# Kernel tuning notes

Hardware: AMD Instinct MI355X
Metric: run time of the kernel (lower is better)

## Reference

```python
import jax, jax.numpy as jnp
import numpy as np

S = 16   # num_states
C = 8    # input_channels
B = 64   # batch
L = 4096 # sequence length


def hyperbolic_sigmoid(x):
    return x / (1 + jnp.abs(x)) * 0.5 + 0.5


def hyperbolic_softmax(logits, axis):
    x = hyperbolic_sigmoid(logits)
    return x / jnp.sum(x, axis=axis, keepdims=True)


def setup_inputs() -> dict:
    key = jax.random.key(0)
    k0, k1, k2, k3 = jax.random.split(key, 4)
    return {
        "log_input_probs": jax.random.normal(k0, (B, L, C), dtype=jnp.float32),
        "invh_initial_state_probs": jax.random.normal(k1, (S,), dtype=jnp.float32),
        "invh_transition_probs": jax.random.normal(k2, (S, C, S), dtype=jnp.float32),
        "invh_accepting_state_probs": jax.random.normal(k3, (S,), dtype=jnp.float32),
    }


def reference(log_input_probs, invh_initial_state_probs, invh_transition_probs, invh_accepting_state_probs):
    # hyperbolic parameterization -> probabilities
    initial_state_probs = hyperbolic_softmax(invh_initial_state_probs, axis=0)         # (S,)
    transition_probs = hyperbolic_softmax(invh_transition_probs, axis=2)               # (S,C,S)
    accepting_state_logprobs = jnp.log(hyperbolic_sigmoid(invh_accepting_state_probs)) # (S,)

    input_probs = jnp.exp(log_input_probs)  # (B,L,C)
    # per-timestep transition matrices, (B,L,S,S)
    trans_each = jnp.einsum('pcn,blc->blpn', transition_probs, input_probs)
    # log-depth chain product m0 @ m1 @ ... @ m_{L-1} via associative scan
    prefix = jax.lax.associative_scan(jnp.matmul, trans_each, axis=1)
    transition_overall = prefix[:, -1]  # (B,S,S)
    # p_state[b,n] = sum_p overall[b,p,n] * init[p]
    p_state = jnp.einsum('bpn,p->bn', transition_overall, initial_state_probs)
    log_p_state = jnp.log(p_state + 1e-20)
    log_acceptance = jax.nn.logsumexp(log_p_state + accepting_state_logprobs[None, :], axis=1)  # (B,)
    return log_acceptance[None]  # (1,B)
```

## Files before the change

### kernel.cpp

```cpp
#include <hip/hip_runtime.h>
#include <hip/hip_bf16.h>
#include <math.h>

#define S 16
#define C 8
#define NB 64
#define L 4096
#define K 64
#define LC 64
#define NQ 16

#define SLOT 320
#define RS 20
#define XSS 10

typedef __attribute__((ext_vector_type(8))) short bf16x8;
typedef __attribute__((ext_vector_type(4))) short bf16x4;
typedef __attribute__((ext_vector_type(4))) float f32x4;
typedef unsigned long long ull;

#define WS_INIT 0
#define WS_ACC  64
#define WS_CLOG 512
#define WS_TTT  16896
#define WS_CP   49664

__device__ __forceinline__ float hsig(float x) {
    return x / (1.0f + fabsf(x)) * 0.5f + 0.5f;
}
__device__ __forceinline__ unsigned int f2bf2(float a, float b) {
    __hip_bfloat162 h = __float22bfloat162_rn(make_float2(a, b));
    unsigned int u; __builtin_memcpy(&u, &h, 4); return u;
}
__device__ __forceinline__ unsigned short f2bf(float f) {
    __hip_bfloat16 h = __float2bfloat16(f);
    unsigned short u; __builtin_memcpy(&u, &h, 2); return u;
}

__device__ __forceinline__ f32x4 mfma16(bf16x4 a, bf16x4 b, f32x4 c) {
#if __has_builtin(__builtin_amdgcn_mfma_f32_16x16x16bf16_1k)
    return __builtin_amdgcn_mfma_f32_16x16x16bf16_1k(a, b, c, 0, 0, 0);
#else
    bf16x8 a8 = {a[0], a[1], a[2], a[3], 0, 0, 0, 0};
    bf16x8 b8 = {b[0], b[1], b[2], b[3], 0, 0, 0, 0};
    return __builtin_amdgcn_mfma_f32_16x16x32_bf16(a8, b8, c, 0, 0, 0);
#endif
}

__device__ __forceinline__ bf16x4 ldfrag4(const unsigned short* base, int lane) {
    return *(const bf16x4*)(base + (lane & 15) * RS + (lane >> 4) * 4);
}
__device__ __forceinline__ bf16x4 ldfrag_g4(const unsigned short* base, int lane) {
    return *(const bf16x4*)(base + (lane & 15) * 16 + (lane >> 4) * 4);
}
__device__ __forceinline__ bf16x4 cvt4(f32x4 d) {
    union { unsigned int u[2]; bf16x4 v; } cv;
    cv.u[0] = f2bf2(d[0], d[1]);
    cv.u[1] = f2bf2(d[2], d[3]);
    return cv.v;
}
__device__ __forceinline__ void store16(unsigned short* slot, f32x4 d, int lane, bool odd) {
    int col = lane & 15, quad = lane >> 4;
    if (odd) {
        ull pk = (ull)f2bf2(d[0], d[1]) | ((ull)f2bf2(d[2], d[3]) << 32);
        *(ull*)(slot + col * RS + quad * 4) = pk;
    } else {
#pragma unroll
        for (int r = 0; r < 4; r++) slot[(quad * 4 + r) * RS + col] = f2bf(d[r]);
    }
}

__device__ __forceinline__ f32x4 tree_upper(unsigned short* slots, int lane, int w,
                                            bf16x4 B1a, bf16x4 B1b) {
    f32x4 z = {0.f, 0.f, 0.f, 0.f};
    f32x4 dA = mfma16(ldfrag4(slots + (8 * w) * SLOT, lane), B1a, z);
    store16(slots + (8 * w) * SLOT, dA, lane, false);
    f32x4 dB = mfma16(ldfrag4(slots + (8 * w + 4) * SLOT, lane), B1b, z);
    f32x4 d3 = mfma16(ldfrag4(slots + (8 * w) * SLOT, lane), cvt4(dB), z);
    store16(slots + (8 * w) * SLOT, d3, lane, w & 1);
    __syncthreads();
    f32x4 root = z;
    if (w == 0) {
        f32x4 d4a = mfma16(ldfrag4(slots, lane), ldfrag4(slots + 8 * SLOT, lane), z);
        f32x4 d4b = mfma16(ldfrag4(slots + 16 * SLOT, lane), ldfrag4(slots + 24 * SLOT, lane), z);
        store16(slots, d4a, lane, false);
        root = mfma16(ldfrag4(slots, lane), cvt4(d4b), z);
    }
    return root;
}

__global__ void __launch_bounds__(256) prepall_kernel(const float* __restrict__ invh_init,
                                                      const float* __restrict__ invh_T,
                                                      const float* __restrict__ invh_acc,
                                                      unsigned char* __restrict__ wsb) {
    __shared__ float Tn[2048];
    int t = threadIdx.x;
    int cc = blockIdx.x, c = cc >> 3, c2 = cc & 7;
    if (t < S * C) {
        float v[S]; float s = 0.f;
#pragma unroll
        for (int n = 0; n < S; n++) { v[n] = hsig(invh_T[t * S + n]); s += v[n]; }
        float inv = 1.f / s;
#pragma unroll
        for (int n = 0; n < S; n++) Tn[t * S + n] = v[n] * inv;
    }
    __syncthreads();
    int p = t >> 4, n = t & 15;
    float a = 0.f;
#pragma unroll
    for (int k = 0; k < S; k++) a += Tn[(p * 8 + c) * 16 + k] * Tn[(k * 8 + c2) * 16 + n];
    ((unsigned short*)(wsb + WS_TTT))[t * 64 + cc] = f2bf(a);

    if (cc == 0 && t < S) {
        float s = 0.f;
#pragma unroll
        for (int k = 0; k < S; k++) s += hsig(invh_init[k]);
        ((float*)(wsb + WS_INIT))[t] = hsig(invh_init[t]) / s;
        ((float*)(wsb + WS_ACC))[t] = logf(hsig(invh_acc[t]));
    }
}

__global__ void __launch_bounds__(256) chunk_kernel(const float* __restrict__ logx,
                                                    unsigned char* __restrict__ wsb) {
    __shared__ __align__(16) unsigned short slots[32 * SLOT];
    __shared__ __align__(16) float xs[LC * XSS];
    __shared__ float clpart[4];

    int tid = threadIdx.x, lane = tid & 63, w = tid >> 6;
    int col = lane & 15, quad = lane >> 4;
    int qi = blockIdx.x, b = blockIdx.y;
    int chunk0 = 4 * qi;

    const unsigned short* TTT = (const unsigned short*)(wsb + WS_TTT);
    bf16x8 bfr[4][2];
#pragma unroll
    for (int jj = 0; jj < 4; jj++) {
        int t = 4 * w + jj;
#pragma unroll
        for (int kk = 0; kk < 2; kk++)
            bfr[jj][kk] = *(const bf16x8*)(TTT + (t * 16 + col) * 64 + kk * 32 + quad * 8);
    }

    const float* xg = logx + ((size_t)b * L + (size_t)chunk0 * LC) * C;
    float2 vv0 = *(const float2*)(xg + 2 * tid);
    float2 vv1 = *(const float2*)(xg + 1 * LC * C + 2 * tid);
    float2 vv2 = *(const float2*)(xg + 2 * LC * C + 2 * tid);
    float2 vv3 = *(const float2*)(xg + 3 * LC * C + 2 * tid);

    f32x4 r0, r1, r2, r3;
#pragma unroll
    for (int ch = 0; ch < 4; ch++) {
        int chunk = chunk0 + ch;

        float2 v = (ch == 0) ? vv0 : (ch == 1) ? vv1 : (ch == 2) ? vv2 : vv3;
        float m = fmaxf(v.x, v.y);
        m = fmaxf(m, __shfl_xor(m, 1));
        m = fmaxf(m, __shfl_xor(m, 2));
        float e0 = __expf(v.x - m), e1 = __expf(v.y - m);
        float s = e0 + e1;
        s += __shfl_xor(s, 1);
        s += __shfl_xor(s, 2);
        float inv = 1.0f / s;
        *(float2*)(xs + (tid >> 2) * XSS + 2 * (tid & 3)) = make_float2(e0 * inv, e1 * inv);
        float lx = ((tid & 3) == 0) ? (m + __logf(s)) : 0.f;
#pragma unroll
        for (int d = 1; d < 64; d <<= 1) lx += __shfl_xor(lx, d);
        if (lane == 0) clpart[w] = lx;
        __syncthreads();
        if (tid == 0)
            ((float*)(wsb + WS_CLOG))[b * K + chunk] = clpart[0] + clpart[1] + clpart[2] + clpart[3];

        bf16x8 afr[2][2];
#pragma unroll
        for (int mt = 0; mt < 2; mt++) {
            int i2 = 2 * (mt * 16 + col);
            const float2* x1p = (const float2*)(xs + (i2 + 1) * XSS);
            float2 q0 = x1p[0], q1 = x1p[1], q2 = x1p[2], q3 = x1p[3];
#pragma unroll
            for (int kk = 0; kk < 2; kk++) {
                float x0 = xs[i2 * XSS + kk * 4 + quad];
                union { unsigned int u[4]; bf16x8 v8; } cv;
                cv.u[0] = f2bf2(x0 * q0.x, x0 * q0.y);
                cv.u[1] = f2bf2(x0 * q1.x, x0 * q1.y);
                cv.u[2] = f2bf2(x0 * q2.x, x0 * q2.y);
                cv.u[3] = f2bf2(x0 * q3.x, x0 * q3.y);
                afr[mt][kk] = cv.v8;
            }
        }

#pragma unroll
        for (int mt = 0; mt < 2; mt++)
#pragma unroll
            for (int jj = 0; jj < 4; jj++) {
                f32x4 acc = {0.f, 0.f, 0.f, 0.f};
#pragma unroll
                for (int kk = 0; kk < 2; kk++)
                    acc = __builtin_amdgcn_mfma_f32_16x16x32_bf16(afr[mt][kk], bfr[jj][kk], acc, 0, 0, 0);
                int t = 4 * w + jj;
#pragma unroll
                for (int r = 0; r < 4; r++) {
                    int i = mt * 16 + quad * 4 + r;
                    int off = (i & 1) ? (col * RS + t) : (t * RS + col);
                    slots[i * SLOT + off] = f2bf(acc[r]);
                }
            }
        __syncthreads();

        bf16x4 B1[2];
        {
            f32x4 z = {0.f, 0.f, 0.f, 0.f};
#pragma unroll
            for (int i2 = 0; i2 < 4; i2++) {
                int i = 4 * w + i2;
                f32x4 d = mfma16(ldfrag4(slots + (2 * i) * SLOT, lane),
                                 ldfrag4(slots + (2 * i + 1) * SLOT, lane), z);
                if (i2 & 1) B1[i2 >> 1] = cvt4(d);
                else store16(slots + (2 * i) * SLOT, d, lane, false);
            }
        }
        f32x4 root = tree_upper(slots, lane, w, B1[0], B1[1]);
        if (ch == 0) r0 = root; else if (ch == 1) r1 = root;
        else if (ch == 2) r2 = root; else r3 = root;
    }

    if (w == 0) {
        f32x4 z = {0.f, 0.f, 0.f, 0.f};
        store16(slots, r0, lane, false);
        f32x4 p01 = mfma16(ldfrag4(slots, lane), cvt4(r1), z);
        store16(slots + 8 * SLOT, r2, lane, false);
        f32x4 p23 = mfma16(ldfrag4(slots + 8 * SLOT, lane), cvt4(r3), z);
        store16(slots, p01, lane, false);
        f32x4 fin = mfma16(ldfrag4(slots, lane), cvt4(p23), z);
        unsigned short* cp = (unsigned short*)(wsb + WS_CP) + ((size_t)b * NQ + qi) * 256;
        if (qi & 1) {
            ull pk = (ull)f2bf2(fin[0], fin[1]) | ((ull)f2bf2(fin[2], fin[3]) << 32);
            *(ull*)(cp + col * 16 + quad * 4) = pk;
        } else {
#pragma unroll
            for (int r = 0; r < 4; r++) cp[(quad * 4 + r) * 16 + col] = f2bf(fin[r]);
        }
    }
}

__global__ void __launch_bounds__(256) reduce_kernel(unsigned char* __restrict__ wsb,
                                                     float* __restrict__ out) {
    __shared__ __align__(16) unsigned short slots[32 * SLOT];
    int tid = threadIdx.x, lane = tid & 63, w = tid >> 6;
    int col = lane & 15, quad = lane >> 4;
    int b = blockIdx.x;

    const unsigned short* cpb = (const unsigned short*)(wsb + WS_CP) + (size_t)b * NQ * 256;
    bf16x4 e0 = ldfrag_g4(cpb + (size_t)(4 * w + 0) * 256, lane);
    bf16x4 e1 = ldfrag_g4(cpb + (size_t)(4 * w + 2) * 256, lane);
    bf16x4 B1a = ldfrag_g4(cpb + (size_t)(4 * w + 1) * 256, lane);
    bf16x4 B1b = ldfrag_g4(cpb + (size_t)(4 * w + 3) * 256, lane);
    *(bf16x4*)(slots + (8 * w) * SLOT + col * RS + quad * 4) = e0;
    *(bf16x4*)(slots + (8 * w + 4) * SLOT + col * RS + quad * 4) = e1;
    f32x4 troot = tree_upper(slots, lane, w, B1a, B1b);

    if (w == 0) {
        const float* initp = (const float*)(wsb + WS_INIT);
        const float* acclog = (const float*)(wsb + WS_ACC);
        float part = 0.f;
#pragma unroll
        for (int r = 0; r < 4; r++) part += initp[quad * 4 + r] * troot[r];
        part += __shfl_xor(part, 16);
        part += __shfl_xor(part, 32);
        float lp = logf(fmaxf(part, 0.f) + 1e-30f) + acclog[col];
        float mx = lp;
#pragma unroll
        for (int d = 1; d < 16; d <<= 1) mx = fmaxf(mx, __shfl_xor(mx, d));
        float a2 = isfinite(mx) ? mx : 0.0f;
        float sm = expf(lp - a2);
#pragma unroll
        for (int d = 1; d < 16; d <<= 1) sm += __shfl_xor(sm, d);
        float cl = ((const float*)(wsb + WS_CLOG))[b * K + lane];
#pragma unroll
        for (int d = 1; d < 64; d <<= 1) cl += __shfl_xor(cl, d);
        if (lane == 0) out[b] = logf(sm) + a2 + cl;
    }
}

extern "C" void kernel_launch(void* const* d_in, const int* in_sizes, int n_in,
                              void* d_out, int out_size, void* d_ws, size_t ws_size,
                              hipStream_t stream) {
    const float* logx = (const float*)d_in[0];
    const float* init = (const float*)d_in[1];
    const float* T    = (const float*)d_in[2];
    const float* acc  = (const float*)d_in[3];
    unsigned char* wsb = (unsigned char*)d_ws;
    float* out = (float*)d_out;

    prepall_kernel<<<64, 256, 0, stream>>>(init, T, acc, wsb);
    chunk_kernel<<<dim3(NQ, NB), 256, 0, stream>>>(logx, wsb);
    reduce_kernel<<<NB, 256, 0, stream>>>(wsb, out);
}
```

Measured before the change: 81.67 us.

## Fuse parameter prep kernel into chunk and reduce kernels, recompute pair matrices per block

Removes the separate prepall kernel launch. Each chunk block now normalizes the transition parameters itself and builds the pairwise products T_c·T_c2 with MFMA into shared memory before loading its B fragments. The reduce kernel computes the initial and accepting probabilities inline. This saves a launch and the dependency on the prep kernel, at the cost of redundant per-block work, more shared memory, and extra syncs. It also adds a launch bound of 4 blocks per CU.

```diff
diff --git a/kernel.cpp b/kernel.cpp
--- a/kernel.cpp
+++ b/kernel.cpp
@@ -13,17 +13,15 @@
 #define SLOT 320
 #define RS 20
 #define XSS 10
+#define TST 40
 
 typedef __attribute__((ext_vector_type(8))) short bf16x8;
 typedef __attribute__((ext_vector_type(4))) short bf16x4;
 typedef __attribute__((ext_vector_type(4))) float f32x4;
 typedef unsigned long long ull;
 
-#define WS_INIT 0
-#define WS_ACC  64
-#define WS_CLOG 512
-#define WS_TTT  16896
-#define WS_CP   49664
+#define WS_CLOG 0
+#define WS_CP   16384
 
 __device__ __forceinline__ float hsig(float x) {
     return x / (1.0f + fabsf(x)) * 0.5f + 0.5f;
@@ -89,40 +87,12 @@
     return root;
 }
 
-__global__ void __launch_bounds__(256) prepall_kernel(const float* __restrict__ invh_init,
-                                                      const float* __restrict__ invh_T,
-                                                      const float* __restrict__ invh_acc,
-                                                      unsigned char* __restrict__ wsb) {
-    __shared__ float Tn[2048];
-    int t = threadIdx.x;
-    int cc = blockIdx.x, c = cc >> 3, c2 = cc & 7;
-    if (t < S * C) {
-        float v[S]; float s = 0.f;
-#pragma unroll
-        for (int n = 0; n < S; n++) { v[n] = hsig(invh_T[t * S + n]); s += v[n]; }
-        float inv = 1.f / s;
-#pragma unroll
-        for (int n = 0; n < S; n++) Tn[t * S + n] = v[n] * inv;
-    }
-    __syncthreads();
-    int p = t >> 4, n = t & 15;
-    float a = 0.f;
-#pragma unroll
-    for (int k = 0; k < S; k++) a += Tn[(p * 8 + c) * 16 + k] * Tn[(k * 8 + c2) * 16 + n];
-    ((unsigned short*)(wsb + WS_TTT))[t * 64 + cc] = f2bf(a);
-
-    if (cc == 0 && t < S) {
-        float s = 0.f;
-#pragma unroll
-        for (int k = 0; k < S; k++) s += hsig(invh_init[k]);
-        ((float*)(wsb + WS_INIT))[t] = hsig(invh_init[t]) / s;
-        ((float*)(wsb + WS_ACC))[t] = logf(hsig(invh_acc[t]));
-    }
-}
-
-__global__ void __launch_bounds__(256) chunk_kernel(const float* __restrict__ logx,
-                                                    unsigned char* __restrict__ wsb) {
+__global__ void __launch_bounds__(256, 4) chunk_kernel(const float* __restrict__ logx,
+                                                       const float* __restrict__ invh_T,
+                                                       unsigned char* __restrict__ wsb) {
     __shared__ __align__(16) unsigned short slots[32 * SLOT];
+    __shared__ __align__(16) unsigned short Arm[128 * RS];
+    __shared__ __align__(16) unsigned short Tcm2[16 * 136];
     __shared__ __align__(16) float xs[LC * XSS];
     __shared__ float clpart[4];
 
@@ -130,22 +100,62 @@
     int col = lane & 15, quad = lane >> 4;
     int qi = blockIdx.x, b = blockIdx.y;
     int chunk0 = 4 * qi;
-
-    const unsigned short* TTT = (const unsigned short*)(wsb + WS_TTT);
-    bf16x8 bfr[4][2];
-#pragma unroll
-    for (int jj = 0; jj < 4; jj++) {
-        int t = 4 * w + jj;
-#pragma unroll
-        for (int kk = 0; kk < 2; kk++)
-            bfr[jj][kk] = *(const bf16x8*)(TTT + (t * 16 + col) * 64 + kk * 32 + quad * 8);
-    }
 
     const float* xg = logx + ((size_t)b * L + (size_t)chunk0 * LC) * C;
     float2 vv0 = *(const float2*)(xg + 2 * tid);
     float2 vv1 = *(const float2*)(xg + 1 * LC * C + 2 * tid);
     float2 vv2 = *(const float2*)(xg + 2 * LC * C + 2 * tid);
     float2 vv3 = *(const float2*)(xg + 3 * LC * C + 2 * tid);
+
+    {
+        const float4* tg = (const float4*)invh_T + tid * 2;
+        float4 aa = tg[0], bb = tg[1];
+        float va0 = hsig(aa.x), va1 = hsig(aa.y), va2 = hsig(aa.z), va3 = hsig(aa.w);
+        float va4 = hsig(bb.x), va5 = hsig(bb.y), va6 = hsig(bb.z), va7 = hsig(bb.w);
+        float s = ((va0 + va1) + (va2 + va3)) + ((va4 + va5) + (va6 + va7));
+        s += __shfl_xor(s, 1);
+        float inv = 1.f / s;
+        unsigned int q01 = f2bf2(va0 * inv, va1 * inv), q23 = f2bf2(va2 * inv, va3 * inv);
+        unsigned int q45 = f2bf2(va4 * inv, va5 * inv), q67 = f2bf2(va6 * inv, va7 * inv);
+        int r = tid >> 1, h = tid & 1, p = r >> 3, c = r & 7;
+        *(ull*)(Arm + r * RS + 8 * h) = (ull)q01 | ((ull)q23 << 32);
+        *(ull*)(Arm + r * RS + 8 * h + 4) = (ull)q45 | ((ull)q67 << 32);
+        unsigned short vb[8] = {(unsigned short)q01, (unsigned short)(q01 >> 16),
+                                (unsigned short)q23, (unsigned short)(q23 >> 16),
+                                (unsigned short)q45, (unsigned short)(q45 >> 16),
+                                (unsigned short)q67, (unsigned short)(q67 >> 16)};
+#pragma unroll
+        for (int i = 0; i < 8; i++) Tcm2[(8 * h + i) * 136 + c * 16 + p] = vb[i];
+    }
+    __syncthreads();
+
+    bf16x8 bfr[4][2];
+    unsigned short* TTTL = slots;
+#pragma unroll
+    for (int kk = 0; kk < 2; kk++) {
+        int c = kk * 4 + w;
+        bf16x4 Af = *(const bf16x4*)(Arm + (col * 8 + c) * RS + quad * 4);
+        f32x4 z = {0.f, 0.f, 0.f, 0.f};
+#pragma unroll
+        for (int cp = 0; cp < 8; cp++) {
+            bf16x4 Bf = *(const bf16x4*)(Tcm2 + col * 136 + cp * 16 + quad * 4);
+            f32x4 d = mfma16(Af, Bf, z);
+#pragma unroll
+            for (int r = 0; r < 4; r++) {
+                int row = (quad * 4 + r) * 16 + col;
+                int blk = w ^ ((row >> 2) & 3);
+                TTTL[row * TST + blk * 8 + cp] = f2bf(d[r]);
+            }
+        }
+        __syncthreads();
+#pragma unroll
+        for (int jj = 0; jj < 4; jj++) {
+            int row = (4 * w + jj) * 16 + col;
+            int blk = quad ^ ((row >> 2) & 3);
+            bfr[jj][kk] = *(const bf16x8*)(TTTL + row * TST + blk * 8);
+        }
+        __syncthreads();
+    }
 
     f32x4 r0, r1, r2, r3;
 #pragma unroll
@@ -243,6 +253,8 @@
 }
 
 __global__ void __launch_bounds__(256) reduce_kernel(unsigned char* __restrict__ wsb,
+                                                     const float* __restrict__ invh_init,
+                                                     const float* __restrict__ invh_acc,
                                                      float* __restrict__ out) {
     __shared__ __align__(16) unsigned short slots[32 * SLOT];
     int tid = threadIdx.x, lane = tid & 63, w = tid >> 6;
@@ -259,14 +271,16 @@
     f32x4 troot = tree_upper(slots, lane, w, B1a, B1b);
 
     if (w == 0) {
-        const float* initp = (const float*)(wsb + WS_INIT);
-        const float* acclog = (const float*)(wsb + WS_ACC);
+        float si = 0.f;
+#pragma unroll
+        for (int k = 0; k < S; k++) si += hsig(invh_init[k]);
+        float isi = 1.f / si;
         float part = 0.f;
 #pragma unroll
-        for (int r = 0; r < 4; r++) part += initp[quad * 4 + r] * troot[r];
+        for (int r = 0; r < 4; r++) part += hsig(invh_init[quad * 4 + r]) * isi * troot[r];
         part += __shfl_xor(part, 16);
         part += __shfl_xor(part, 32);
-        float lp = logf(fmaxf(part, 0.f) + 1e-30f) + acclog[col];
+        float lp = logf(fmaxf(part, 0.f) + 1e-30f) + logf(hsig(invh_acc[col]));
         float mx = lp;
 #pragma unroll
         for (int d = 1; d < 16; d <<= 1) mx = fmaxf(mx, __shfl_xor(mx, d));
@@ -291,7 +305,6 @@
     unsigned char* wsb = (unsigned char*)d_ws;
     float* out = (float*)d_out;
 
-    prepall_kernel<<<64, 256, 0, stream>>>(init, T, acc, wsb);
-    chunk_kernel<<<dim3(NQ, NB), 256, 0, stream>>>(logx, wsb);
-    reduce_kernel<<<NB, 256, 0, stream>>>(wsb, out);
-}
+    chunk_kernel<<<dim3(NQ, NB), 256, 0, stream>>>(logx, T, wsb);
+    reduce_kernel<<<NB, 256, 0, stream>>>(wsb, init, acc, out);
+}
```

Measured after the change: 87.56 us. 1.07x slower.
